# Optimization experiments

Measured on AMD Instinct MI355X. Metric: run time of the kernel, lower is better.

Reference implementation:

```python
import jax, jax.numpy as jnp
import numpy as np

H = 768          # low-res grid side
S = 3            # scale_factor -> output is (H*S, H*S)
HID = 32         # hidden_channels
N = H * H


def _grid_edges(h):
    """8-neighbor directed edge list, same as create_graph's python loop."""
    idx = np.arange(h * h, dtype=np.int32).reshape(h, h)
    srcs, dsts = [], []
    for di in (-1, 0, 1):
        for dj in (-1, 0, 1):
            if di == 0 and dj == 0:
                continue
            rs = slice(max(0, -di), h - max(0, di))
            cs = slice(max(0, -dj), h - max(0, dj))
            rd = slice(max(0, di), h - max(0, -di))
            cd = slice(max(0, dj), h - max(0, -dj))
            srcs.append(idx[rs, cs].ravel())
            dsts.append(idx[rd, cd].ravel())
    return np.stack([np.concatenate(srcs), np.concatenate(dsts)])


def setup_inputs() -> dict:
    key = jax.random.key(0)
    ks = jax.random.split(key, 4)
    edge_index = jnp.asarray(_grid_edges(H))  # [2, E] int32
    x = jax.random.normal(ks[0], (N, 3), dtype=jnp.float32)
    W1 = jax.random.normal(ks[1], (3, HID), dtype=jnp.float32) * (1.0 / np.sqrt(3))
    W2 = jax.random.normal(ks[2], (HID, HID), dtype=jnp.float32) * (1.0 / np.sqrt(HID))
    W3 = jax.random.normal(ks[3], (HID, S * S), dtype=jnp.float32) * (1.0 / np.sqrt(HID))
    return {
        "x": x, "edge_index": edge_index,
        "W1": W1, "b1": jnp.zeros((HID,), jnp.float32),
        "W2": W2, "b2": jnp.zeros((HID,), jnp.float32),
        "W3": W3, "b3": jnp.zeros((S * S,), jnp.float32),
    }


def _gcn_layer(h, W, b, src, dst, norm_e, self_norm, n):
    # GCNConv: x' = D^-1/2 (A + I) D^-1/2 (x W) + b
    h = h @ W
    msg = h[src] * norm_e[:, None]                        # gather + normalize
    agg = jax.ops.segment_sum(msg, dst, num_segments=n)    # scatter-add
    return agg + h * self_norm[:, None] + b                # self-loop + bias


def reference(x, edge_index, W1, b1, W2, b2, W3, b3):
    n = x.shape[0]
    src, dst = edge_index[0], edge_index[1]
    # degrees with self-loops (PyG gcn_norm: deg on target col, +1 self loop)
    deg = jax.ops.segment_sum(jnp.ones(src.shape, jnp.float32), dst, num_segments=n) + 1.0
    dinv = jax.lax.rsqrt(deg)
    norm_e = dinv[src] * dinv[dst]
    self_norm = dinv * dinv

    h = jax.nn.relu(_gcn_layer(x, W1, b1, src, dst, norm_e, self_norm, n))
    h = jax.nn.relu(_gcn_layer(h, W2, b2, src, dst, norm_e, self_norm, n))
    h = _gcn_layer(h, W3, b3, src, dst, norm_e, self_norm, n)

    # pixel-shuffle reshape: [N, S*S] -> [1, H*S, H*S]
    out = h.reshape(1, H, H, S, S).transpose(0, 1, 3, 2, 4).reshape(1, H * S, H * S)
    return out
```

## Files before the change

### kernel.cpp

```cpp
#include <hip/hip_runtime.h>


constexpr int HH = 768, SS = 3;
constexpr int TI = 12, TJ = 24;
constexpr int NBJ = 32;
constexpr int NT = 512;

constexpr int G0C = 30;  constexpr int N0  = 540;
constexpr int S0C = 28;  constexpr int NS0 = 448;
constexpr int R3C = 26;  constexpr int NS1 = 364;
constexpr int NS1P = 368;
constexpr int ON  = 288;

constexpr int G0O = 0;
constexpr int G1A = 0;
constexpr int G1B = 896;
constexpr int S1P = 2176;
constexpr int D3O = 8064;
constexpr int SMEMF = 8432;

constexpr int TB0 = 0;
constexpr int TB1 = 1472;
constexpr int TB2 = 2944;
constexpr int OUT0 = 3328;
constexpr int OUT1 = 4480;
constexpr int OUT2 = 5632;

#define SWZ(row) ((((row) >> 1) & 3) << 2)

typedef _Float16 f16x8 __attribute__((ext_vector_type(8)));
typedef float    f32x4 __attribute__((ext_vector_type(4)));
using h2 = decltype(__builtin_amdgcn_cvt_pkrtz(0.f, 0.f));

#define PK(a, b)  __builtin_amdgcn_cvt_pkrtz((a), (b))
#define BC2(u)    __builtin_bit_cast(h2, (u))
#define BCU(x)    __builtin_bit_cast(uint32_t, (x))
#define MFMA16(a, b, c) __builtin_amdgcn_mfma_f32_16x16x32_f16((a), (b), (c), 0, 0, 0)

__device__ __forceinline__ float dinv_of(int gi, int gj) {
    int e = (1 + (gi > 0) + (gi < HH - 1)) * (1 + (gj > 0) + (gj < HH - 1));
    return e == 9 ? 0.33333334f : (e == 6 ? 0.40824829f : 0.5f);
}
__device__ __forceinline__ void add4(float4& a, const float4 v) {
    a.x += v.x; a.y += v.y; a.z += v.z; a.w += v.w;
}
#define FMA4G(acc, s, wp) { const float4 _w = *(const float4*)(wp); \
    acc.x += (s) * _w.x; acc.y += (s) * _w.y; acc.z += (s) * _w.z; acc.w += (s) * _w.w; }

__global__ __launch_bounds__(NT, 8) void gnn_fused(
    const float* __restrict__ x,
    const float* __restrict__ W1, const float* __restrict__ b1,
    const float* __restrict__ W2, const float* __restrict__ b2,
    const float* __restrict__ W3, const float* __restrict__ b3,
    float* __restrict__ out)
{
    __shared__ __align__(16) float smem[SMEMF];
    const int tid = threadIdx.x;
    const int lane = tid & 63, wid = tid >> 6;
    const int lr = lane & 15, lg = lane >> 4;
    const int bi = blockIdx.x / NBJ;
    const int bj = blockIdx.x % NBJ;
    const int oi = bi * TI, oj = bj * TJ;

    for (int n = tid; n < N0; n += NT) {
        int li = n / G0C, lj = n - li * G0C;
        int gi = oi - 3 + li, gj = oj - 3 + lj;
        float4 v = {0.f, 0.f, 0.f, 0.f};
        if ((unsigned)gi < HH && (unsigned)gj < HH) {
            float d = dinv_of(gi, gj);
            const float* xp = x + 3 * ((size_t)gi * HH + gj);
            v.x = d * xp[0]; v.y = d * xp[1]; v.z = d * xp[2];
        }
        *(float4*)&smem[G0O + n * 4] = v;
    }
    if (tid < NS1P) {
        float v = 0.f;
        if (tid < NS1) {
            int li = tid / R3C, lj = tid - li * R3C;
            int gi = oi - 1 + li, gj = oj - 1 + lj;
            if ((unsigned)gi < HH && (unsigned)gj < HH) v = dinv_of(gi, gj);
        }
        smem[D3O + tid] = v;
    }
    if (tid < 64)
        smem[S1P + NS1 * 16 + tid] = 0.f;
    __syncthreads();

    float4 s0a = {0,0,0,0};
    float d2a = 0.f;
    if (tid < NS0) {
        int li = tid / S0C, lj = tid - li * S0C;
        int base = li * G0C + lj;
        #pragma unroll
        for (int di = 0; di < 3; ++di)
            #pragma unroll
            for (int dj = 0; dj < 3; ++dj)
                add4(s0a, *(const float4*)&smem[G0O + (base + di * G0C + dj) * 4]);
        int gi = oi - 2 + li, gj = oj - 2 + lj;
        if ((unsigned)gi < HH && (unsigned)gj < HH) d2a = dinv_of(gi, gj);
    }
    const int fli = tid / R3C, flj = tid - fli * R3C;
    const int fbase = fli * S0C + flj;
    __syncthreads();

    #define MM1Q(q, BUF) \
        if (tid < NS0) { \
            float4 a = {0,0,0,0}; \
            FMA4G(a, s0a.x, W1 + 4 * (q)) FMA4G(a, s0a.y, W1 + 32 + 4 * (q)) FMA4G(a, s0a.z, W1 + 64 + 4 * (q)) \
            const float4 bb = *(const float4*)&b1[4 * (q)]; \
            float gx = d2a * fmaxf(d2a * a.x + bb.x, 0.f); \
            float gy = d2a * fmaxf(d2a * a.y + bb.y, 0.f); \
            float gz = d2a * fmaxf(d2a * a.z + bb.z, 0.f); \
            float gw = d2a * fmaxf(d2a * a.w + bb.w, 0.f); \
            uint2 u; u.x = BCU(PK(gx, gy)); u.y = BCU(PK(gz, gw)); \
            *(uint2*)&smem[(BUF) + tid * 2] = u; \
        }

    #define BS2Q(q, BUF) \
        if (tid < NS1) { \
            const int _tb = (BUF) + fbase * 2; \
            const uint2 u00 = *(const uint2*)&smem[_tb + 0]; \
            const uint2 u01 = *(const uint2*)&smem[_tb + 2]; \
            const uint2 u02 = *(const uint2*)&smem[_tb + 4]; \
            const uint2 u10 = *(const uint2*)&smem[_tb + 2 * S0C + 0]; \
            const uint2 u11 = *(const uint2*)&smem[_tb + 2 * S0C + 2]; \
            const uint2 u12 = *(const uint2*)&smem[_tb + 2 * S0C + 4]; \
            const uint2 u20 = *(const uint2*)&smem[_tb + 4 * S0C + 0]; \
            const uint2 u21 = *(const uint2*)&smem[_tb + 4 * S0C + 2]; \
            const uint2 u22 = *(const uint2*)&smem[_tb + 4 * S0C + 4]; \
            h2 rl0 = (BC2(u00.x) + BC2(u01.x)) + BC2(u02.x); \
            h2 rl1 = (BC2(u10.x) + BC2(u11.x)) + BC2(u12.x); \
            h2 rl2 = (BC2(u20.x) + BC2(u21.x)) + BC2(u22.x); \
            h2 sl  = (rl0 + rl1) + rl2; \
            h2 rh0 = (BC2(u00.y) + BC2(u01.y)) + BC2(u02.y); \
            h2 rh1 = (BC2(u10.y) + BC2(u11.y)) + BC2(u12.y); \
            h2 rh2 = (BC2(u20.y) + BC2(u21.y)) + BC2(u22.y); \
            h2 sh  = (rh0 + rh1) + rh2; \
            uint2 uo; uo.x = BCU(sl); uo.y = BCU(sh); \
            *(uint2*)&smem[S1P + tid * 16 + (2 * (q) ^ SWZ(tid))] = uo; \
        }

    MM1Q(0, G1A) __syncthreads();
    BS2Q(0, G1A) MM1Q(1, G1B) __syncthreads();
    BS2Q(1, G1B) MM1Q(2, G1A) __syncthreads();
    BS2Q(2, G1A) MM1Q(3, G1B) __syncthreads();
    BS2Q(3, G1B) MM1Q(4, G1A) __syncthreads();
    BS2Q(4, G1A) MM1Q(5, G1B) __syncthreads();
    BS2Q(5, G1B) MM1Q(6, G1A) __syncthreads();
    BS2Q(6, G1A) MM1Q(7, G1B) __syncthreads();
    BS2Q(7, G1B)

    uint4 uw20, uw21, uw3;
    {
        const int k0 = 8 * lg;
        uw20.x = BCU(PK(W2[(k0+0)*32 + lr],      W2[(k0+1)*32 + lr]));
        uw20.y = BCU(PK(W2[(k0+2)*32 + lr],      W2[(k0+3)*32 + lr]));
        uw20.z = BCU(PK(W2[(k0+4)*32 + lr],      W2[(k0+5)*32 + lr]));
        uw20.w = BCU(PK(W2[(k0+6)*32 + lr],      W2[(k0+7)*32 + lr]));
        uw21.x = BCU(PK(W2[(k0+0)*32 + 16 + lr], W2[(k0+1)*32 + 16 + lr]));
        uw21.y = BCU(PK(W2[(k0+2)*32 + 16 + lr], W2[(k0+3)*32 + 16 + lr]));
        uw21.z = BCU(PK(W2[(k0+4)*32 + 16 + lr], W2[(k0+5)*32 + 16 + lr]));
        uw21.w = BCU(PK(W2[(k0+6)*32 + 16 + lr], W2[(k0+7)*32 + 16 + lr]));
        float a0w=0.f,b0w=0.f,a1w=0.f,b1w=0.f,a2w=0.f,b2w=0.f,a3w=0.f,b3w=0.f;
        if (lr < 9) {
            a0w = W3[(k0+0)*9 + lr]; b0w = W3[(k0+1)*9 + lr];
            a1w = W3[(k0+2)*9 + lr]; b1w = W3[(k0+3)*9 + lr];
            a2w = W3[(k0+4)*9 + lr]; b2w = W3[(k0+5)*9 + lr];
            a3w = W3[(k0+6)*9 + lr]; b3w = W3[(k0+7)*9 + lr];
        }
        uw3.x = BCU(PK(a0w, b0w)); uw3.y = BCU(PK(a1w, b1w));
        uw3.z = BCU(PK(a2w, b2w)); uw3.w = BCU(PK(a3w, b3w));
    }
    const float b2c0 = b2[lr], b2c1 = b2[16 + lr];
    __syncthreads();

    const f16x8 bw20 = __builtin_bit_cast(f16x8, uw20);
    const f16x8 bw21 = __builtin_bit_cast(f16x8, uw21);
    const f16x8 bw3  = __builtin_bit_cast(f16x8, uw3);
    _Float16* hp = (_Float16*)smem;

    #define ACT1(dv, c0r, c1r, rr) { \
        const float dd_ = (dv); \
        float h0 = dd_ * fmaxf(dd_ * (c0r) + b2c0, 0.f); \
        float h1 = dd_ * fmaxf(dd_ * (c1r) + b2c1, 0.f); \
        const int row_ = nb + (rr); \
        const int sz_ = SWZ(row_); \
        hp[2 * (S1P + row_ * 16 + ((lr >> 1) ^ sz_)) + (lr & 1)] = (_Float16)h0; \
        hp[2 * (S1P + row_ * 16 + ((8 + (lr >> 1)) ^ sz_)) + (lr & 1)] = (_Float16)h1; }

    #define AFRAG(rt) __builtin_bit_cast(f16x8, \
        *(const uint4*)&smem[S1P + ((rt) * 16 + lr) * 16 + (4 * lg ^ SWZ((rt) * 16 + lr))])

    #define MM2TILE(rt) { \
        f16x8 aa = AFRAG(rt); \
        f32x4 c0 = {0.f, 0.f, 0.f, 0.f}, c1 = {0.f, 0.f, 0.f, 0.f}; \
        c0 = MFMA16(aa, bw20, c0); \
        c1 = MFMA16(aa, bw21, c1); \
        const int nb = (rt) * 16 + lg * 4; \
        const float4 dd = *(const float4*)&smem[D3O + nb]; \
        ACT1(dd.x, c0[0], c1[0], 0) \
        ACT1(dd.y, c0[1], c1[1], 1) \
        ACT1(dd.z, c0[2], c1[2], 2) \
        ACT1(dd.w, c0[3], c1[3], 3) }

    MM2TILE(wid)
    MM2TILE(wid + 8)
    if (wid < 7) { MM2TILE(wid + 16) }
    __syncthreads();

    f16x8 a30 = AFRAG(wid);
    f16x8 a31 = AFRAG(wid + 8);
    f16x8 a32 = a30;
    if (wid < 7) a32 = AFRAG(wid + 16);
    __syncthreads();

    #define MM3TILE(rt, af) { \
        f32x4 tt = {0.f, 0.f, 0.f, 0.f}; \
        tt = MFMA16((af), bw3, tt); \
        const int nb = (rt) * 16 + lg * 4; \
        if (lr < 4) { \
            smem[TB0 + (nb + 0) * 4 + lr] = tt[0]; \
            smem[TB0 + (nb + 1) * 4 + lr] = tt[1]; \
            smem[TB0 + (nb + 2) * 4 + lr] = tt[2]; \
            smem[TB0 + (nb + 3) * 4 + lr] = tt[3]; \
        } else if (lr < 8) { \
            smem[TB1 + (nb + 0) * 4 + lr - 4] = tt[0]; \
            smem[TB1 + (nb + 1) * 4 + lr - 4] = tt[1]; \
            smem[TB1 + (nb + 2) * 4 + lr - 4] = tt[2]; \
            smem[TB1 + (nb + 3) * 4 + lr - 4] = tt[3]; \
        } else if (lr == 8) { \
            smem[TB2 + nb + 0] = tt[0]; \
            smem[TB2 + nb + 1] = tt[1]; \
            smem[TB2 + nb + 2] = tt[2]; \
            smem[TB2 + nb + 3] = tt[3]; } }

    MM3TILE(wid, a30)
    MM3TILE(wid + 8, a31)
    if (wid < 7) { MM3TILE(wid + 16, a32) }
    __syncthreads();

    for (int item = tid; item < 3 * ON; item += NT) {
        int p = item / ON, n = item - p * ON;
        int li = n / TJ, lj = n - li * TJ;
        int src = li * R3C + lj;
        float d = dinv_of(oi + li, oj + lj);
        if (p == 2) {
            float s = 0.f;
            #pragma unroll
            for (int di = 0; di < 3; ++di)
                #pragma unroll
                for (int dj = 0; dj < 3; ++dj)
                    s += smem[TB2 + src + di * R3C + dj];
            smem[OUT2 + n] = d * s + b3[8];
        } else {
            const int tb = p ? TB1 : TB0;
            float4 s = {0.f, 0.f, 0.f, 0.f};
            #pragma unroll
            for (int di = 0; di < 3; ++di)
                #pragma unroll
                for (int dj = 0; dj < 3; ++dj)
                    add4(s, *(const float4*)&smem[tb + (src + di * R3C + dj) * 4]);
            const float4 bb = *(const float4*)&b3[4 * p];
            float4 o;
            o.x = d * s.x + bb.x; o.y = d * s.y + bb.y;
            o.z = d * s.z + bb.z; o.w = d * s.w + bb.w;
            *(float4*)&smem[(p ? OUT1 : OUT0) + n * 4] = o;
        }
    }
    __syncthreads();

    #define ORD(n, c) ((c) < 8 ? smem[((c) < 4 ? OUT0 : OUT1) + (n) * 4 + ((c) & 3)] \
                               : smem[OUT2 + (n)])
    for (int q = tid; q < 36 * 18; q += NT) {
        int rr = q / 18, cc0 = 4 * (q % 18);
        int ii = rr / 3, si = rr - 3 * ii;
        float4 o;
        { int cc = cc0 + 0, jj = cc / 3, sj = cc - 3 * jj; o.x = ORD(ii * TJ + jj, si * 3 + sj); }
        { int cc = cc0 + 1, jj = cc / 3, sj = cc - 3 * jj; o.y = ORD(ii * TJ + jj, si * 3 + sj); }
        { int cc = cc0 + 2, jj = cc / 3, sj = cc - 3 * jj; o.z = ORD(ii * TJ + jj, si * 3 + sj); }
        { int cc = cc0 + 3, jj = cc / 3, sj = cc - 3 * jj; o.w = ORD(ii * TJ + jj, si * 3 + sj); }
        *(float4*)&out[(size_t)(oi * SS + rr) * (HH * SS) + oj * SS + cc0] = o;
    }
}

extern "C" void kernel_launch(void* const* d_in, const int* in_sizes, int n_in,
                              void* d_out, int out_size, void* d_ws, size_t ws_size,
                              hipStream_t stream) {
    const float* x  = (const float*)d_in[0];
    const float* W1 = (const float*)d_in[2];
    const float* b1 = (const float*)d_in[3];
    const float* W2 = (const float*)d_in[4];
    const float* b2 = (const float*)d_in[5];
    const float* W3 = (const float*)d_in[6];
    const float* b3 = (const float*)d_in[7];
    float* out = (float*)d_out;

    gnn_fused<<<dim3(64 * NBJ), dim3(NT), 0, stream>>>(x, W1, b1, W2, b2, W3, b3, out);
}
```

Before: 40.25 us.

## Fuse layer-2 neighbor sum directly into MFMA A-fragment loads

Layer-1 activations for all 32 channels are now computed in one pass per node and stored as a swizzled fp16 row. The 3x3 neighbor sum is then done per lane while building the MFMA A fragment, instead of through eight ping-pong quarter-channel stages with a barrier each. This removes about seven __syncthreads and the intermediate S1 buffer, which shrinks shared memory. In exchange it needs more registers (16 packed words per thread) and does redundant fragment-row reads, and the out-of-range rows for tile wid+16 now read the aliased region without explicit zero padding.

```diff
diff --git a/kernel.cpp b/kernel.cpp
--- a/kernel.cpp
+++ b/kernel.cpp
@@ -12,12 +12,9 @@
 constexpr int NS1P = 368;
 constexpr int ON  = 288;
 
-constexpr int G0O = 0;
-constexpr int G1A = 0;
-constexpr int G1B = 896;
-constexpr int S1P = 2176;
-constexpr int D3O = 8064;
-constexpr int SMEMF = 8432;
+constexpr int G1O = 0;
+constexpr int D3O = 7168;
+constexpr int SMEMF = 7536;
 
 constexpr int TB0 = 0;
 constexpr int TB1 = 1472;
@@ -71,7 +68,7 @@
             const float* xp = x + 3 * ((size_t)gi * HH + gj);
             v.x = d * xp[0]; v.y = d * xp[1]; v.z = d * xp[2];
         }
-        *(float4*)&smem[G0O + n * 4] = v;
+        *(float4*)&smem[G1O + n * 4] = v;
     }
     if (tid < NS1P) {
         float v = 0.f;
@@ -82,8 +79,6 @@
         }
         smem[D3O + tid] = v;
     }
-    if (tid < 64)
-        smem[S1P + NS1 * 16 + tid] = 0.f;
     __syncthreads();
 
     float4 s0a = {0,0,0,0};
@@ -95,60 +90,17 @@
         for (int di = 0; di < 3; ++di)
             #pragma unroll
             for (int dj = 0; dj < 3; ++dj)
-                add4(s0a, *(const float4*)&smem[G0O + (base + di * G0C + dj) * 4]);
+                add4(s0a, *(const float4*)&smem[G1O + (base + di * G0C + dj) * 4]);
         int gi = oi - 2 + li, gj = oj - 2 + lj;
         if ((unsigned)gi < HH && (unsigned)gj < HH) d2a = dinv_of(gi, gj);
     }
-    const int fli = tid / R3C, flj = tid - fli * R3C;
-    const int fbase = fli * S0C + flj;
-    __syncthreads();
-
-    #define MM1Q(q, BUF) \
-        if (tid < NS0) { \
-            float4 a = {0,0,0,0}; \
-            FMA4G(a, s0a.x, W1 + 4 * (q)) FMA4G(a, s0a.y, W1 + 32 + 4 * (q)) FMA4G(a, s0a.z, W1 + 64 + 4 * (q)) \
-            const float4 bb = *(const float4*)&b1[4 * (q)]; \
-            float gx = d2a * fmaxf(d2a * a.x + bb.x, 0.f); \
-            float gy = d2a * fmaxf(d2a * a.y + bb.y, 0.f); \
-            float gz = d2a * fmaxf(d2a * a.z + bb.z, 0.f); \
-            float gw = d2a * fmaxf(d2a * a.w + bb.w, 0.f); \
-            uint2 u; u.x = BCU(PK(gx, gy)); u.y = BCU(PK(gz, gw)); \
-            *(uint2*)&smem[(BUF) + tid * 2] = u; \
-        }
-
-    #define BS2Q(q, BUF) \
-        if (tid < NS1) { \
-            const int _tb = (BUF) + fbase * 2; \
-            const uint2 u00 = *(const uint2*)&smem[_tb + 0]; \
-            const uint2 u01 = *(const uint2*)&smem[_tb + 2]; \
-            const uint2 u02 = *(const uint2*)&smem[_tb + 4]; \
-            const uint2 u10 = *(const uint2*)&smem[_tb + 2 * S0C + 0]; \
-            const uint2 u11 = *(const uint2*)&smem[_tb + 2 * S0C + 2]; \
-            const uint2 u12 = *(const uint2*)&smem[_tb + 2 * S0C + 4]; \
-            const uint2 u20 = *(const uint2*)&smem[_tb + 4 * S0C + 0]; \
-            const uint2 u21 = *(const uint2*)&smem[_tb + 4 * S0C + 2]; \
-            const uint2 u22 = *(const uint2*)&smem[_tb + 4 * S0C + 4]; \
-            h2 rl0 = (BC2(u00.x) + BC2(u01.x)) + BC2(u02.x); \
-            h2 rl1 = (BC2(u10.x) + BC2(u11.x)) + BC2(u12.x); \
-            h2 rl2 = (BC2(u20.x) + BC2(u21.x)) + BC2(u22.x); \
-            h2 sl  = (rl0 + rl1) + rl2; \
-            h2 rh0 = (BC2(u00.y) + BC2(u01.y)) + BC2(u02.y); \
-            h2 rh1 = (BC2(u10.y) + BC2(u11.y)) + BC2(u12.y); \
-            h2 rh2 = (BC2(u20.y) + BC2(u21.y)) + BC2(u22.y); \
-            h2 sh  = (rh0 + rh1) + rh2; \
-            uint2 uo; uo.x = BCU(sl); uo.y = BCU(sh); \
-            *(uint2*)&smem[S1P + tid * 16 + (2 * (q) ^ SWZ(tid))] = uo; \
-        }
-
-    MM1Q(0, G1A) __syncthreads();
-    BS2Q(0, G1A) MM1Q(1, G1B) __syncthreads();
-    BS2Q(1, G1B) MM1Q(2, G1A) __syncthreads();
-    BS2Q(2, G1A) MM1Q(3, G1B) __syncthreads();
-    BS2Q(3, G1B) MM1Q(4, G1A) __syncthreads();
-    BS2Q(4, G1A) MM1Q(5, G1B) __syncthreads();
-    BS2Q(5, G1B) MM1Q(6, G1A) __syncthreads();
-    BS2Q(6, G1A) MM1Q(7, G1B) __syncthreads();
-    BS2Q(7, G1B)
+    const int nA0 = wid * 16 + lr;
+    const int nA1 = (wid + 8) * 16 + lr;
+    const int nA2 = (wid + 16) * 16 + lr;
+    const int fb0 = (nA0 / R3C) * S0C + (nA0 % R3C);
+    const int fb1 = (nA1 / R3C) * S0C + (nA1 % R3C);
+    const int fb2 = (nA2 / R3C) * S0C + (nA2 % R3C);
+    __syncthreads();
 
     uint4 uw20, uw21, uw3;
     {
@@ -172,42 +124,87 @@
         uw3.z = BCU(PK(a2w, b2w)); uw3.w = BCU(PK(a3w, b3w));
     }
     const float b2c0 = b2[lr], b2c1 = b2[16 + lr];
+
+    if (tid < NS0) {
+        uint32_t g[16];
+        #pragma unroll
+        for (int q = 0; q < 8; ++q) {
+            float4 a = {0,0,0,0};
+            FMA4G(a, s0a.x, W1 + 4 * q)
+            FMA4G(a, s0a.y, W1 + 32 + 4 * q)
+            FMA4G(a, s0a.z, W1 + 64 + 4 * q)
+            const float4 bb = *(const float4*)&b1[4 * q];
+            float gx = d2a * fmaxf(d2a * a.x + bb.x, 0.f);
+            float gy = d2a * fmaxf(d2a * a.y + bb.y, 0.f);
+            float gz = d2a * fmaxf(d2a * a.z + bb.z, 0.f);
+            float gw = d2a * fmaxf(d2a * a.w + bb.w, 0.f);
+            g[2 * q]     = BCU(PK(gx, gy));
+            g[2 * q + 1] = BCU(PK(gz, gw));
+        }
+        const int sz = SWZ(tid);
+        uint4 u;
+        u.x = g[0];  u.y = g[1];  u.z = g[2];  u.w = g[3];
+        *(uint4*)&smem[G1O + tid * 16 + (0 ^ sz)] = u;
+        u.x = g[4];  u.y = g[5];  u.z = g[6];  u.w = g[7];
+        *(uint4*)&smem[G1O + tid * 16 + (4 ^ sz)] = u;
+        u.x = g[8];  u.y = g[9];  u.z = g[10]; u.w = g[11];
+        *(uint4*)&smem[G1O + tid * 16 + (8 ^ sz)] = u;
+        u.x = g[12]; u.y = g[13]; u.z = g[14]; u.w = g[15];
+        *(uint4*)&smem[G1O + tid * 16 + (12 ^ sz)] = u;
+    }
     __syncthreads();
 
     const f16x8 bw20 = __builtin_bit_cast(f16x8, uw20);
     const f16x8 bw21 = __builtin_bit_cast(f16x8, uw21);
     const f16x8 bw3  = __builtin_bit_cast(f16x8, uw3);
+
+    #define TAP(rr) (*(const uint4*)&smem[G1O + (rr) * 16 + ((4 * lg) ^ SWZ(rr))])
+    #define ROWSUM(rr, o0, o1, o2) { \
+        const uint4 va = TAP((rr)+(o0)); const uint4 vb = TAP((rr)+(o1)); const uint4 vc = TAP((rr)+(o2)); \
+        r0 = (BC2(va.x) + BC2(vb.x)) + BC2(vc.x); \
+        r1 = (BC2(va.y) + BC2(vb.y)) + BC2(vc.y); \
+        r2 = (BC2(va.z) + BC2(vb.z)) + BC2(vc.z); \
+        r3 = (BC2(va.w) + BC2(vb.w)) + BC2(vc.w); }
+
+    #define BS2MM2(fb, cc0, cc1) { \
+        h2 r0, r1, r2, r3, s0_, s1_, s2_, s3_; \
+        ROWSUM((fb), 0, 1, 2)               s0_ = r0; s1_ = r1; s2_ = r2; s3_ = r3; \
+        ROWSUM((fb) + S0C, 0, 1, 2)         s0_ += r0; s1_ += r1; s2_ += r2; s3_ += r3; \
+        ROWSUM((fb) + 2 * S0C, 0, 1, 2)     s0_ += r0; s1_ += r1; s2_ += r2; s3_ += r3; \
+        uint4 af_; af_.x = BCU(s0_); af_.y = BCU(s1_); af_.z = BCU(s2_); af_.w = BCU(s3_); \
+        const f16x8 aa_ = __builtin_bit_cast(f16x8, af_); \
+        cc0 = MFMA16(aa_, bw20, cc0); \
+        cc1 = MFMA16(aa_, bw21, cc1); }
+
+    f32x4 c00 = {0,0,0,0}, c01 = {0,0,0,0};
+    f32x4 c10 = {0,0,0,0}, c11 = {0,0,0,0};
+    f32x4 c20 = {0,0,0,0}, c21 = {0,0,0,0};
+    BS2MM2(fb0, c00, c01)
+    BS2MM2(fb1, c10, c11)
+    if (wid < 7) { BS2MM2(fb2, c20, c21) }
+    __syncthreads();
+
     _Float16* hp = (_Float16*)smem;
-
-    #define ACT1(dv, c0r, c1r, rr) { \
-        const float dd_ = (dv); \
-        float h0 = dd_ * fmaxf(dd_ * (c0r) + b2c0, 0.f); \
-        float h1 = dd_ * fmaxf(dd_ * (c1r) + b2c1, 0.f); \
-        const int row_ = nb + (rr); \
-        const int sz_ = SWZ(row_); \
-        hp[2 * (S1P + row_ * 16 + ((lr >> 1) ^ sz_)) + (lr & 1)] = (_Float16)h0; \
-        hp[2 * (S1P + row_ * 16 + ((8 + (lr >> 1)) ^ sz_)) + (lr & 1)] = (_Float16)h1; }
-
-    #define AFRAG(rt) __builtin_bit_cast(f16x8, \
-        *(const uint4*)&smem[S1P + ((rt) * 16 + lr) * 16 + (4 * lg ^ SWZ((rt) * 16 + lr))])
-
-    #define MM2TILE(rt) { \
-        f16x8 aa = AFRAG(rt); \
-        f32x4 c0 = {0.f, 0.f, 0.f, 0.f}, c1 = {0.f, 0.f, 0.f, 0.f}; \
-        c0 = MFMA16(aa, bw20, c0); \
-        c1 = MFMA16(aa, bw21, c1); \
+    #define WRH(rt, cc0, cc1) { \
         const int nb = (rt) * 16 + lg * 4; \
         const float4 dd = *(const float4*)&smem[D3O + nb]; \
-        ACT1(dd.x, c0[0], c1[0], 0) \
-        ACT1(dd.y, c0[1], c1[1], 1) \
-        ACT1(dd.z, c0[2], c1[2], 2) \
-        ACT1(dd.w, c0[3], c1[3], 3) }
-
-    MM2TILE(wid)
-    MM2TILE(wid + 8)
-    if (wid < 7) { MM2TILE(wid + 16) }
-    __syncthreads();
-
+        _Pragma("unroll") \
+        for (int r = 0; r < 4; ++r) { \
+            const float dv = r == 0 ? dd.x : (r == 1 ? dd.y : (r == 2 ? dd.z : dd.w)); \
+            const float h0 = dv * fmaxf(dv * cc0[r] + b2c0, 0.f); \
+            const float h1 = dv * fmaxf(dv * cc1[r] + b2c1, 0.f); \
+            const int row_ = nb + r; \
+            const int sz_ = SWZ(row_); \
+            hp[2 * (G1O + row_ * 16 + (((lr >> 1)) ^ sz_)) + (lr & 1)] = (_Float16)h0; \
+            hp[2 * (G1O + row_ * 16 + ((8 + (lr >> 1)) ^ sz_)) + (lr & 1)] = (_Float16)h1; } }
+
+    WRH(wid, c00, c01)
+    WRH(wid + 8, c10, c11)
+    if (wid < 7) { WRH(wid + 16, c20, c21) }
+    __syncthreads();
+
+    #define AFRAG(rt) __builtin_bit_cast(f16x8, \
+        *(const uint4*)&smem[G1O + ((rt) * 16 + lr) * 16 + ((4 * lg) ^ SWZ((rt) * 16 + lr))])
     f16x8 a30 = AFRAG(wid);
     f16x8 a31 = AFRAG(wid + 8);
     f16x8 a32 = a30;
```

After: 38.38 us. 1.05x faster.
